# Performance work log

Measured on AMD Instinct MI355X. Metric: run time of the kernel, lower is better.

The kernel has to match this reference:

```python
import jax, jax.numpy as jnp
import numpy as np

E = 640000   # number of scattered rows (edges)
N = 50000    # number of segments / attention keys
V = 128      # values_dim
K = 128      # keys_dim


def setup_inputs() -> dict:
    key = jax.random.key(0)
    k1, k2, k3, k4, k5 = jax.random.split(key, 5)
    scattered_values = jax.random.normal(k1, (E, V), dtype=jnp.float32)
    indices = jax.random.randint(k2, (E,), 0, N)
    attn_keys = jax.random.normal(k3, (N, K), dtype=jnp.float32)
    # nn.Linear(keys_dim, values_dim): weight [V, K], bias [V]
    lim = 1.0 / np.sqrt(K)
    W = jax.random.uniform(k4, (V, K), minval=-lim, maxval=lim, dtype=jnp.float32)
    b = jax.random.uniform(k5, (V,), minval=-lim, maxval=lim, dtype=jnp.float32)
    return {"scattered_values": scattered_values, "indices": indices,
            "attn_keys": attn_keys, "W": W, "b": b}


def reference(scattered_values, indices, attn_keys, W, b):
    # Project keys: [N, K] @ [K, V] + [V] -> [N, V]
    keys_proj = jnp.einsum('nk,vk->nv', attn_keys, W) + b
    # Gather projected key for each scattered row: [E, V]
    gathered = keys_proj[indices]
    # Per-row attention logit: [E]
    probs = jnp.sum(scattered_values * gathered, axis=1)
    # Segment (scatter) softmax over rows sharing the same index
    seg_max = jax.ops.segment_max(probs, indices, num_segments=N)
    ex = jnp.exp(probs - seg_max[indices])
    denom = jax.ops.segment_sum(ex, indices, num_segments=N)
    scores = ex / denom[indices]                      # [E]
    # Weighted segment-sum aggregation: [N, V]
    attn_applied = jax.ops.segment_sum(scattered_values * scores[:, None],
                                       indices, num_segments=N)
    return scores, attn_applied
```

## Files before the change

kernel.cpp:

```cpp
#include <hip/hip_runtime.h>
#include <cstdint>

#define DIM 128
#define CAP 64

__global__ __launch_bounds__(256) void hist_kernel(const int* __restrict__ idx,
                                                   int* __restrict__ count,
                                                   int* __restrict__ bucket,
                                                   int E) {
  int e = blockIdx.x * 256 + threadIdx.x;
  if (e >= E) return;
  int n = idx[e];
  int r = atomicAdd(&count[n], 1);
  if (r < CAP) bucket[n * CAP + r] = e;
}

__global__ __launch_bounds__(256) void keys_proj_gemm(const float* __restrict__ A,
                                                      const float* __restrict__ W,
                                                      const float* __restrict__ bias,
                                                      float* __restrict__ C,
                                                      int Nrows) {
  __shared__ float As[16][128];
  __shared__ float Ws[16][128];
  int t = threadIdx.x;
  int tx = t & 15;
  int ty = t >> 4;
  int n0 = blockIdx.x * 128;

  float acc[8][8];
#pragma unroll
  for (int r = 0; r < 8; ++r)
#pragma unroll
    for (int c = 0; c < 8; ++c) acc[r][c] = 0.f;

  for (int k0 = 0; k0 < DIM; k0 += 16) {
#pragma unroll
    for (int i = 0; i < 2; ++i) {
      int f = t + i * 256;
      int n = f >> 2;
      int kq = f & 3;
      int gn = n0 + n;
      if (gn >= Nrows) gn = Nrows - 1;
      const float4 a4 = *(const float4*)(A + (size_t)gn * DIM + k0 + kq * 4);
      As[kq * 4 + 0][n] = a4.x; As[kq * 4 + 1][n] = a4.y;
      As[kq * 4 + 2][n] = a4.z; As[kq * 4 + 3][n] = a4.w;
      const float4 w4 = *(const float4*)(W + (size_t)n * DIM + k0 + kq * 4);
      Ws[kq * 4 + 0][n] = w4.x; Ws[kq * 4 + 1][n] = w4.y;
      Ws[kq * 4 + 2][n] = w4.z; Ws[kq * 4 + 3][n] = w4.w;
    }
    __syncthreads();
#pragma unroll
    for (int kk = 0; kk < 16; ++kk) {
      float av[8], wv[8];
      *(float4*)&av[0] = *(const float4*)&As[kk][ty * 8];
      *(float4*)&av[4] = *(const float4*)&As[kk][ty * 8 + 4];
      *(float4*)&wv[0] = *(const float4*)&Ws[kk][tx * 8];
      *(float4*)&wv[4] = *(const float4*)&Ws[kk][tx * 8 + 4];
#pragma unroll
      for (int r = 0; r < 8; ++r)
#pragma unroll
        for (int c = 0; c < 8; ++c)
          acc[r][c] = fmaf(av[r], wv[c], acc[r][c]);
    }
    __syncthreads();
  }

#pragma unroll
  for (int r = 0; r < 8; ++r) {
    int gn = n0 + ty * 8 + r;
    if (gn < Nrows) {
#pragma unroll
      for (int c = 0; c < 8; c += 4) {
        int v = tx * 8 + c;
        float4 o;
        o.x = acc[r][c + 0] + bias[v + 0];
        o.y = acc[r][c + 1] + bias[v + 1];
        o.z = acc[r][c + 2] + bias[v + 2];
        o.w = acc[r][c + 3] + bias[v + 3];
        *(float4*)(C + (size_t)gn * DIM + v) = o;
      }
    }
  }
}

__global__ __launch_bounds__(256) void seg_attn_kernel(const float* __restrict__ sv,
                                                       const int* __restrict__ count,
                                                       const int* __restrict__ bucket,
                                                       const float* __restrict__ kp,
                                                       float* __restrict__ scores,
                                                       float* __restrict__ attn,
                                                       int Nseg) {
  int gw = (blockIdx.x * 256 + threadIdx.x) >> 6;
  int lane = threadIdx.x & 63;
  if (gw >= Nseg) return;
  int n = gw;
  int cnt = count[n];
  cnt = cnt > CAP ? CAP : cnt;
  int g = lane >> 4;
  int q = lane & 15;

  const float4* kprow = (const float4*)(kp + (size_t)n * DIM);
  float4 kpa = kprow[q * 2 + 0];
  float4 kpb = kprow[q * 2 + 1];

  int e_lane = (lane < cnt) ? bucket[n * CAP + lane] : 0;

  int iters = (cnt + 3) >> 2;
  float psave = 0.f;
  float m_g = -3.4e38f;
  float l_g = 0.f;
  float4 O0 = {0.f, 0.f, 0.f, 0.f};
  float4 O1 = {0.f, 0.f, 0.f, 0.f};

  for (int j = 0; j < iters; ++j) {
    int ei = 4 * j + g;
    bool valid = ei < cnt;
    int e = __shfl(e_lane, ei);
    const float4* src = (const float4*)(sv + (size_t)e * DIM) + q * 2;
    float4 a0 = src[0];
    float4 a1 = src[1];
    float d = a0.x * kpa.x + a0.y * kpa.y + a0.z * kpa.z + a0.w * kpa.w
            + a1.x * kpb.x + a1.y * kpb.y + a1.z * kpb.z + a1.w * kpb.w;
    d += __shfl_xor(d, 1);
    d += __shfl_xor(d, 2);
    d += __shfl_xor(d, 4);
    d += __shfl_xor(d, 8);
    if (!valid) d = -3.4e38f;
    if (q == j) psave = d;

    float mn = fmaxf(m_g, d);
    float factor = __expf(m_g - mn);
    float w = valid ? __expf(d - mn) : 0.f;
    l_g = fmaf(l_g, factor, w);
    O0.x = fmaf(O0.x, factor, w * a0.x); O0.y = fmaf(O0.y, factor, w * a0.y);
    O0.z = fmaf(O0.z, factor, w * a0.z); O0.w = fmaf(O0.w, factor, w * a0.w);
    O1.x = fmaf(O1.x, factor, w * a1.x); O1.y = fmaf(O1.y, factor, w * a1.y);
    O1.z = fmaf(O1.z, factor, w * a1.z); O1.w = fmaf(O1.w, factor, w * a1.w);
    m_g = mn;
  }

  float M = m_g;
  M = fmaxf(M, __shfl_xor(M, 16));
  M = fmaxf(M, __shfl_xor(M, 32));
  float scale = __expf(m_g - M);

  float denom = l_g * scale;
  denom += __shfl_xor(denom, 16);
  denom += __shfl_xor(denom, 32);
  float rinv = denom > 0.f ? __frcp_rn(denom) : 0.f;

  float p_lane = __shfl(psave, (lane & 3) * 16 + (lane >> 2));
  if (lane < cnt) scores[e_lane] = __expf(p_lane - M) * rinv;

  O0.x *= scale; O0.y *= scale; O0.z *= scale; O0.w *= scale;
  O1.x *= scale; O1.y *= scale; O1.z *= scale; O1.w *= scale;
#pragma unroll
  for (int mask = 16; mask < 64; mask <<= 1) {
    O0.x += __shfl_xor(O0.x, mask); O0.y += __shfl_xor(O0.y, mask);
    O0.z += __shfl_xor(O0.z, mask); O0.w += __shfl_xor(O0.w, mask);
    O1.x += __shfl_xor(O1.x, mask); O1.y += __shfl_xor(O1.y, mask);
    O1.z += __shfl_xor(O1.z, mask); O1.w += __shfl_xor(O1.w, mask);
  }
  if (g == 0) {
    float4 o0 = O0, o1 = O1;
    o0.x *= rinv; o0.y *= rinv; o0.z *= rinv; o0.w *= rinv;
    o1.x *= rinv; o1.y *= rinv; o1.z *= rinv; o1.w *= rinv;
    float4* dst = (float4*)(attn + (size_t)n * DIM) + q * 2;
    dst[0] = o0;
    dst[1] = o1;
  }
}

extern "C" void kernel_launch(void* const* d_in, const int* in_sizes, int n_in,
                              void* d_out, int out_size, void* d_ws, size_t ws_size,
                              hipStream_t stream) {
  const float* sv   = (const float*)d_in[0];
  const int*   idx  = (const int*)d_in[1];
  const float* A    = (const float*)d_in[2];
  const float* W    = (const float*)d_in[3];
  const float* bias = (const float*)d_in[4];

  const int E = in_sizes[1];
  const int N = in_sizes[2] / DIM;

  float* scores = (float*)d_out;
  float* attn   = (float*)d_out + E;

  char* ws = (char*)d_ws;
  size_t off_bucket = ((size_t)N * 4 + 255) & ~(size_t)255;
  size_t off_kp     = off_bucket + (size_t)N * CAP * 4;
  int*   count  = (int*)ws;
  int*   bucket = (int*)(ws + off_bucket);
  float* kp     = (float*)(ws + off_kp);

  hipMemsetAsync(count, 0, (size_t)N * 4, stream);

  hist_kernel<<<(E + 255) / 256, 256, 0, stream>>>(idx, count, bucket, E);
  keys_proj_gemm<<<(N + 127) / 128, 256, 0, stream>>>(A, W, bias, kp, N);
  seg_attn_kernel<<<(N + 3) / 4, 256, 0, stream>>>(sv, count, bucket, kp,
                                                   scores, attn, N);
}
```

Before: 536.1 us.

## Fuse histogram and key projection into one launch; prefetch rows in segment attention

Merges the histogram/bucketing kernel and the key-projection GEMM into a single launch, with block ranges split by role, so the two independent stages can run concurrently and one launch is saved. The GEMM tile shrinks from 128 to 64 rows, giving more blocks for parallelism at the cost of reloading W more often. The segment attention loop now software-prefetches the next group of scattered rows into registers to hide gather latency, which uses more registers.

```diff
diff --git a/kernel.cpp b/kernel.cpp
--- a/kernel.cpp
+++ b/kernel.cpp
@@ -4,60 +4,64 @@
 #define DIM 128
 #define CAP 64
 
-__global__ __launch_bounds__(256) void hist_kernel(const int* __restrict__ idx,
-                                                   int* __restrict__ count,
-                                                   int* __restrict__ bucket,
-                                                   int E) {
-  int e = blockIdx.x * 256 + threadIdx.x;
-  if (e >= E) return;
-  int n = idx[e];
-  int r = atomicAdd(&count[n], 1);
-  if (r < CAP) bucket[n * CAP + r] = e;
-}
-
-__global__ __launch_bounds__(256) void keys_proj_gemm(const float* __restrict__ A,
-                                                      const float* __restrict__ W,
-                                                      const float* __restrict__ bias,
-                                                      float* __restrict__ C,
-                                                      int Nrows) {
-  __shared__ float As[16][128];
+__global__ __launch_bounds__(256) void fused_hist_gemm(
+    const int* __restrict__ idx, int* __restrict__ count, int* __restrict__ bucket, int E,
+    const float* __restrict__ A, const float* __restrict__ W,
+    const float* __restrict__ bias, float* __restrict__ C, int Nrows,
+    int gemmBlocks) {
+  __shared__ float As[16][64];
   __shared__ float Ws[16][128];
+
   int t = threadIdx.x;
+
+  if (blockIdx.x >= gemmBlocks) {
+    int e = (blockIdx.x - gemmBlocks) * 256 + t;
+    if (e < E) {
+      int n = idx[e];
+      int r = atomicAdd(&count[n], 1);
+      if (r < CAP) bucket[n * CAP + r] = e;
+    }
+    return;
+  }
+
   int tx = t & 15;
   int ty = t >> 4;
-  int n0 = blockIdx.x * 128;
-
-  float acc[8][8];
-#pragma unroll
-  for (int r = 0; r < 8; ++r)
+  int n0 = blockIdx.x * 64;
+
+  float acc[4][8];
+#pragma unroll
+  for (int r = 0; r < 4; ++r)
 #pragma unroll
     for (int c = 0; c < 8; ++c) acc[r][c] = 0.f;
 
   for (int k0 = 0; k0 < DIM; k0 += 16) {
-#pragma unroll
-    for (int i = 0; i < 2; ++i) {
-      int f = t + i * 256;
-      int n = f >> 2;
-      int kq = f & 3;
+    {
+      int n = t >> 2;
+      int kq = t & 3;
       int gn = n0 + n;
       if (gn >= Nrows) gn = Nrows - 1;
       const float4 a4 = *(const float4*)(A + (size_t)gn * DIM + k0 + kq * 4);
       As[kq * 4 + 0][n] = a4.x; As[kq * 4 + 1][n] = a4.y;
       As[kq * 4 + 2][n] = a4.z; As[kq * 4 + 3][n] = a4.w;
-      const float4 w4 = *(const float4*)(W + (size_t)n * DIM + k0 + kq * 4);
-      Ws[kq * 4 + 0][n] = w4.x; Ws[kq * 4 + 1][n] = w4.y;
-      Ws[kq * 4 + 2][n] = w4.z; Ws[kq * 4 + 3][n] = w4.w;
+#pragma unroll
+      for (int i = 0; i < 2; ++i) {
+        int f = t + i * 256;
+        int v = f >> 2;
+        int kq2 = f & 3;
+        const float4 w4 = *(const float4*)(W + (size_t)v * DIM + k0 + kq2 * 4);
+        Ws[kq2 * 4 + 0][v] = w4.x; Ws[kq2 * 4 + 1][v] = w4.y;
+        Ws[kq2 * 4 + 2][v] = w4.z; Ws[kq2 * 4 + 3][v] = w4.w;
+      }
     }
     __syncthreads();
 #pragma unroll
     for (int kk = 0; kk < 16; ++kk) {
-      float av[8], wv[8];
-      *(float4*)&av[0] = *(const float4*)&As[kk][ty * 8];
-      *(float4*)&av[4] = *(const float4*)&As[kk][ty * 8 + 4];
+      float av[4], wv[8];
+      *(float4*)&av[0] = *(const float4*)&As[kk][ty * 4];
       *(float4*)&wv[0] = *(const float4*)&Ws[kk][tx * 8];
       *(float4*)&wv[4] = *(const float4*)&Ws[kk][tx * 8 + 4];
 #pragma unroll
-      for (int r = 0; r < 8; ++r)
+      for (int r = 0; r < 4; ++r)
 #pragma unroll
         for (int c = 0; c < 8; ++c)
           acc[r][c] = fmaf(av[r], wv[c], acc[r][c]);
@@ -66,8 +70,8 @@
   }
 
 #pragma unroll
-  for (int r = 0; r < 8; ++r) {
-    int gn = n0 + ty * 8 + r;
+  for (int r = 0; r < 4; ++r) {
+    int gn = n0 + ty * 4 + r;
     if (gn < Nrows) {
 #pragma unroll
       for (int c = 0; c < 8; c += 4) {
@@ -112,13 +116,25 @@
   float4 O0 = {0.f, 0.f, 0.f, 0.f};
   float4 O1 = {0.f, 0.f, 0.f, 0.f};
 
+  float4 a0 = {0.f, 0.f, 0.f, 0.f}, a1 = {0.f, 0.f, 0.f, 0.f};
+  if (iters > 0) {
+    int e = __shfl(e_lane, g);
+    const float4* s0 = (const float4*)(sv + (size_t)e * DIM) + q * 2;
+    a0 = s0[0];
+    a1 = s0[1];
+  }
+
   for (int j = 0; j < iters; ++j) {
+    float4 na0 = a0, na1 = a1;
+    if (j + 1 < iters) {
+      int en = __shfl(e_lane, 4 * (j + 1) + g);
+      const float4* sn = (const float4*)(sv + (size_t)en * DIM) + q * 2;
+      na0 = sn[0];
+      na1 = sn[1];
+    }
+
     int ei = 4 * j + g;
     bool valid = ei < cnt;
-    int e = __shfl(e_lane, ei);
-    const float4* src = (const float4*)(sv + (size_t)e * DIM) + q * 2;
-    float4 a0 = src[0];
-    float4 a1 = src[1];
     float d = a0.x * kpa.x + a0.y * kpa.y + a0.z * kpa.z + a0.w * kpa.w
             + a1.x * kpb.x + a1.y * kpb.y + a1.z * kpb.z + a1.w * kpb.w;
     d += __shfl_xor(d, 1);
@@ -137,6 +153,9 @@
     O1.x = fmaf(O1.x, factor, w * a1.x); O1.y = fmaf(O1.y, factor, w * a1.y);
     O1.z = fmaf(O1.z, factor, w * a1.z); O1.w = fmaf(O1.w, factor, w * a1.w);
     m_g = mn;
+
+    a0 = na0;
+    a1 = na1;
   }
 
   float M = m_g;
@@ -195,8 +214,10 @@
 
   hipMemsetAsync(count, 0, (size_t)N * 4, stream);
 
-  hist_kernel<<<(E + 255) / 256, 256, 0, stream>>>(idx, count, bucket, E);
-  keys_proj_gemm<<<(N + 127) / 128, 256, 0, stream>>>(A, W, bias, kp, N);
+  int gemmBlocks = (N + 63) / 64;
+  int histBlocks = (E + 255) / 256;
+  fused_hist_gemm<<<gemmBlocks + histBlocks, 256, 0, stream>>>(
+      idx, count, bucket, E, A, W, bias, kp, N, gemmBlocks);
   seg_attn_kernel<<<(N + 3) / 4, 256, 0, stream>>>(sv, count, bucket, kp,
                                                    scores, attn, N);
 }
```

Result: faster. 516.3 us (-3.7%).
